# Kernel optimization log

Hardware: AMD Instinct MI355X
Metric: run time of the kernel (lower is better)

Reference implementation:

```python
import jax, jax.numpy as jnp
import numpy as np
from jax import lax

# Dimensions
B, CIN, COUT = 8, 3, 3
NF = 128          # num_features
K = 9             # DISCO kernel_shape (number of filter basis functions)
HLAT, WLON = 181, 360   # in_shape == out_shape (1-degree equiangular sphere grid)
KH, KW = 5, 5     # compact lat/lon support of each DISCO basis function


def setup_inputs() -> dict:
    key = jax.random.key(0)
    ks = jax.random.split(key, 10)
    s = lambda fan: 1.0 / np.sqrt(fan)
    return {
        "x": jax.random.normal(ks[0], (B, CIN, HLAT, WLON), jnp.float32),
        # DISCO conv: latitude-dependent basis filters, quadrature weights, channel mix
        "psi": jax.random.normal(ks[1], (K, HLAT, KH, KW), jnp.float32) * s(KH * KW),
        "quad": jnp.abs(jax.random.normal(ks[2], (HLAT,), jnp.float32)) * (1.0 / HLAT)
                + jnp.sin(jnp.pi * (jnp.arange(HLAT) + 0.5) / HLAT) * (1.0 / HLAT),
        "w1": jax.random.normal(ks[3], (NF, CIN, K), jnp.float32) * s(CIN * K),
        "b1": jnp.zeros((NF,), jnp.float32),
        # standard conv2d stages
        "w2": jax.random.normal(ks[4], (NF // 2, NF, 5, 5), jnp.float32) * s(NF * 25),
        "b2": jnp.zeros((NF // 2,), jnp.float32),
        "w3": jax.random.normal(ks[5], (COUT, NF // 2, 5, 5), jnp.float32) * s(NF // 2 * 25),
        "b3": jnp.zeros((COUT,), jnp.float32),
    }


def _disco_conv_s2(x, psi, quad, w, b):
    """Discrete-continuous spherical conv: latitude-dependent gather + weighted sum.
    x: [B,C,H,W]; psi: [K,H,KH,KW]; quad: [H]; w: [O,C,K]; b: [O] -> [B,O,H,W]"""
    H, W = x.shape[-2], x.shape[-1]
    rh, rw = KH // 2, KW // 2
    xw = x * quad[None, None, :, None]                       # quadrature-weighted input
    # neighborhood indices: clipped in latitude, circular in longitude
    hi = jnp.clip(jnp.arange(H)[:, None] + jnp.arange(KH)[None, :] - rh, 0, H - 1)  # [H,KH]
    wi = (jnp.arange(W)[:, None] + jnp.arange(KW)[None, :] - rw) % W                # [W,KW]
    g = xw[:, :, hi, :]                                      # [B,C,H,KH,W]
    patches = g[:, :, :, :, wi]                              # [B,C,H,KH,W,KW]
    # project onto latitude-dependent filter basis, then mix channels per basis
    z = jnp.einsum('khij,bchiwj->bckhw', psi, patches)       # [B,C,K,H,W]
    return jnp.einsum('ock,bckhw->bohw', w, z) + b[None, :, None, None]


def _conv2d(x, w, b, pad):
    y = lax.conv_general_dilated(x, w, (1, 1), [(pad, pad), (pad, pad)],
                                 dimension_numbers=('NCHW', 'OIHW', 'NCHW'))
    return y + b[None, :, None, None]


def reference(x, psi, quad, w1, b1, w2, b2, w3, b3):
    h = jax.nn.relu(_disco_conv_s2(x, psi, quad, w1, b1))
    h = jax.nn.relu(_conv2d(h, w2, b2, 2))
    return _conv2d(h, w3, b3, 2)
```

## Files before the change

kernel.cpp:

```cpp
#include <hip/hip_runtime.h>
#include <hip/hip_bf16.h>

#define HLAT 181
#define WLON 360
#define HW (HLAT * WLON)
#define HPAD 188
#define WPAD 368
#define PCH ((size_t)HPAD * WPAD * 16)
#define W2P 372
#define PLANE2 ((size_t)HPAD * W2P * 64)
#define ZROW ((size_t)12 * 4 * 32 * 16)

typedef __attribute__((ext_vector_type(4)))  short short4v;
typedef __attribute__((ext_vector_type(8)))  short short8v;
typedef __attribute__((ext_vector_type(4)))  float f32x4;
typedef __attribute__((ext_vector_type(16))) float f32x16;

static __device__ __forceinline__ ushort bf16_hi_bits(float f) {
  union { float f; unsigned u; } c; c.f = f;
  unsigned u = c.u;
  unsigned rounded = u + 0x7FFF + ((u >> 16) & 1);
  return (ushort)(rounded >> 16);
}
static __device__ __forceinline__ float bf16_to_f(ushort b) {
  union { unsigned u; float f; } c; c.u = ((unsigned)b) << 16;
  return c.f;
}

__global__ __launch_bounds__(256) void k_tw(const float* __restrict__ w2,
                                            const float* __restrict__ w3,
                                            const float* __restrict__ w1,
                                            const float* __restrict__ b1,
                                            ushort* __restrict__ w2f,
                                            ushort* __restrict__ w1f,
                                            ushort* __restrict__ w3f) {
  int idx = blockIdx.x * 256 + threadIdx.x;
  if (idx < 51200) {
    int l   = idx & 63;
    int p   = (idx >> 6) & 1;
    int m   = (idx >> 7) & 1;
    int ch  = (idx >> 8) & 7;
    int tap = idx >> 11;
    int oc  = m * 32 + (l & 31);
    int ci0 = ch * 16 + (l >> 5) * 8;
#pragma unroll
    for (int j = 0; j < 8; ++j) {
      float f = w2[(oc * 128 + ci0 + j) * 25 + tap];
      ushort hi = bf16_hi_bits(f);
      w2f[(size_t)idx * 8 + j] = (p == 0) ? hi : bf16_hi_bits(f - bf16_to_f(hi));
    }
  }
  if (idx < 1024) {
    int l = idx & 63;
    int e = idx >> 6;
    int p  = e & 1;
    int kc = (e >> 1) & 1;
    int m  = e >> 2;
    int oc = m * 32 + (l & 31);
    int k0 = kc * 16 + (l >> 5) * 8;
#pragma unroll
    for (int j = 0; j < 8; ++j) {
      int k = k0 + j;
      float f = (k < 27) ? w1[oc * 27 + k] : (k == 27 ? b1[oc] : 0.f);
      ushort hi = bf16_hi_bits(f);
      w1f[(size_t)idx * 8 + j] = (p == 0) ? hi : bf16_hi_bits(f - bf16_to_f(hi));
    }
  }
  if (idx < 6400) {
    int l   = idx & 63;
    int p   = (idx >> 6) & 1;
    int kc  = (idx >> 7) & 1;
    int tap = idx >> 8;
    int oc  = l & 15;
    int ci0 = kc * 32 + (l >> 4) * 8;
#pragma unroll
    for (int j = 0; j < 8; ++j) {
      float f = (oc < 3) ? w3[(oc * 64 + ci0 + j) * 25 + tap] : 0.f;
      ushort hi = bf16_hi_bits(f);
      w3f[(size_t)idx * 8 + j] = (p == 0) ? hi : bf16_hi_bits(f - bf16_to_f(hi));
    }
  }
}

__global__ __launch_bounds__(256) void k_zring(ushort* __restrict__ h1s) {
  const int i = blockIdx.x * 256 + threadIdx.x;
  if (i >= 4024) return;
  int row, col;
  if (i < 736)       { row = i / 368;              col = i % 368; }
  else if (i < 2576) { int p = i - 736;  row = 183 + p / 368; col = p % 368; }
  else if (i < 2938) { int p = i - 2576; row = 2 + p % 181;   col = p / 181; }
  else               { int p = i - 2938; row = 2 + p % 181;   col = 362 + p / 181; }
  short8v z = {0, 0, 0, 0, 0, 0, 0, 0};
  short8v* d = (short8v*)(h1s + (size_t)blockIdx.y * PCH + ((size_t)row * 368 + col) * 16);
  d[0] = z; d[1] = z;
}

__global__ __launch_bounds__(256) void k_zring2(ushort* __restrict__ h2p) {
  const int i = blockIdx.x * 256 + threadIdx.x;
  if (i >= 4776) return;
  int row, col;
  if (i < 744)       { row = i / W2P;             col = i % W2P; }
  else if (i < 2604) { int p = i - 744;  row = 183 + p / W2P; col = p % W2P; }
  else               { int p = i - 2604; row = 2 + p % 181;
                       int cI = p / 181; col = (cI < 2) ? cI : 360 + cI; }
  short8v z = {0, 0, 0, 0, 0, 0, 0, 0};
  short8v* d = (short8v*)(h2p + (size_t)blockIdx.y * PLANE2 + ((size_t)row * W2P + col) * 64);
#pragma unroll
  for (int k = 0; k < 8; ++k) d[k] = z;
}

__global__ __launch_bounds__(384, 2) void k_z(const float* __restrict__ x,
    const float* __restrict__ psi, const float* __restrict__ quad,
    ushort* __restrict__ zbuf, int b0) {
  const int h = blockIdx.x;
  const int bi = blockIdx.y;
  const int b = b0 + bi;
  const int tid = threadIdx.x;
  float z[28];
#pragma unroll
  for (int q = 0; q < 28; ++q) z[q] = 0.f;
  if (tid < 360) {
#pragma unroll 1
    for (int i = 0; i < 5; ++i) {
      int hi = h + i - 2;
      hi = hi < 0 ? 0 : (hi >= HLAT ? HLAT - 1 : hi);
      const float qv = quad[hi];
      float pv[45];
#pragma unroll
      for (int kk = 0; kk < 9; ++kk)
#pragma unroll
        for (int j = 0; j < 5; ++j)
          pv[kk * 5 + j] = psi[((size_t)(kk * HLAT + h)) * 25 + i * 5 + j];
#pragma unroll
      for (int c = 0; c < 3; ++c) {
        const float* row = x + ((size_t)(b * 3 + c) * HLAT + hi) * WLON;
        float v[5];
#pragma unroll
        for (int j = 0; j < 5; ++j) {
          int wj = tid + j - 2;
          wj = wj < 0 ? wj + WLON : (wj >= WLON ? wj - WLON : wj);
          v[j] = row[wj] * qv;
        }
#pragma unroll
        for (int kk = 0; kk < 9; ++kk) {
          float a = 0.f;
#pragma unroll
          for (int j = 0; j < 5; ++j) a += pv[kk * 5 + j] * v[j];
          z[c * 9 + kk] += a;
        }
      }
    }
    z[27] = 1.0f;
  }
  ushort hiv[32], lov[32];
#pragma unroll
  for (int q = 0; q < 28; ++q) {
    const ushort hb = bf16_hi_bits(z[q]);
    hiv[q] = hb;
    lov[q] = bf16_hi_bits(z[q] - bf16_to_f(hb));
  }
#pragma unroll
  for (int q = 28; q < 32; ++q) { hiv[q] = 0; lov[q] = 0; }

  ushort* tb = zbuf + (size_t)(bi * HLAT + h) * ZROW +
               (size_t)(tid >> 5) * 2048 + (size_t)(tid & 31) * 16;
#pragma unroll
  for (int pk = 0; pk < 4; ++pk) {
    const ushort* src = (pk < 2 ? hiv : lov) + (pk & 1) * 16;
    union { ushort u[8]; short8v v8; } a0, a1;
#pragma unroll
    for (int j = 0; j < 8; ++j) { a0.u[j] = src[j]; a1.u[j] = src[8 + j]; }
    *(short8v*)(tb + (size_t)pk * 512 + 0) = a0.v8;
    *(short8v*)(tb + (size_t)pk * 512 + 8) = a1.v8;
  }
}

__global__ __launch_bounds__(256, 2) void k_mv(const ushort* __restrict__ zbuf,
    const ushort* __restrict__ w1f, ushort* __restrict__ h1s) {
  __shared__ ushort st[4][16][32][16];
  const int h = blockIdx.x;
  const int bi = blockIdx.y;
  const int tid = threadIdx.x;
  const int wv = tid >> 6;
  const int l = tid & 63;
  const int l31 = l & 31;
  const int q = l >> 5;
  const short8v* wf1 = (const short8v*)w1f;
  short8v A[4][2][2];
#pragma unroll
  for (int m = 0; m < 4; ++m)
#pragma unroll
    for (int kc = 0; kc < 2; ++kc)
#pragma unroll
      for (int p = 0; p < 2; ++p)
        A[m][kc][p] = wf1[(size_t)(((m * 2 + kc) * 2 + p) * 64 + l)];

  ushort* base = h1s + (size_t)bi * 16 * PCH;
  const ushort* zrow = zbuf + (size_t)(bi * HLAT + h) * ZROW;
#pragma unroll
  for (int nn = 0; nn < 3; ++nn) {
    const int n = wv * 3 + nn;
    const ushort* zn = zrow + (size_t)n * 2048 + l31 * 16 + q * 8;
    const short8v bh0 = *(const short8v*)(zn + 0);
    const short8v bh1 = *(const short8v*)(zn + 512);
    const short8v bl0 = *(const short8v*)(zn + 1024);
    const short8v bl1 = *(const short8v*)(zn + 1536);
#pragma unroll
    for (int m = 0; m < 4; ++m) {
      f32x16 acc;
#pragma unroll
      for (int e = 0; e < 16; ++e) acc[e] = 0.f;
      acc = __builtin_amdgcn_mfma_f32_32x32x16_bf16(A[m][0][0], bh0, acc, 0, 0, 0);
      acc = __builtin_amdgcn_mfma_f32_32x32x16_bf16(A[m][0][1], bh0, acc, 0, 0, 0);
      acc = __builtin_amdgcn_mfma_f32_32x32x16_bf16(A[m][0][0], bl0, acc, 0, 0, 0);
      acc = __builtin_amdgcn_mfma_f32_32x32x16_bf16(A[m][1][0], bh1, acc, 0, 0, 0);
      acc = __builtin_amdgcn_mfma_f32_32x32x16_bf16(A[m][1][1], bh1, acc, 0, 0, 0);
      acc = __builtin_amdgcn_mfma_f32_32x32x16_bf16(A[m][1][0], bl1, acc, 0, 0, 0);
#pragma unroll
      for (int r = 0; r < 4; ++r) {
        const int rb = 8 * r + 4 * q;
        const int p2h = m * 2 + (rb >> 4);
        const int ci0 = rb & 15;
        short4v h4, l4;
#pragma unroll
        for (int j = 0; j < 4; ++j) {
          const float v = fmaxf(acc[r * 4 + j], 0.f);
          const ushort hb = bf16_hi_bits(v);
          h4[j] = (short)hb;
          l4[j] = (short)bf16_hi_bits(v - bf16_to_f(hb));
        }
        *(short4v*)&st[wv][p2h][l31][ci0] = h4;
        *(short4v*)&st[wv][8 + p2h][l31][ci0] = l4;
      }
    }
    const int pxr = n * 32 + (l >> 1);
    if (pxr < 360) {
      const size_t po = ((size_t)(h + 2) * WPAD + (pxr + 2)) * 16 + (l & 1) * 8;
#pragma unroll
      for (int p2 = 0; p2 < 16; ++p2) {
        const short8v v = *(const short8v*)&st[wv][p2][l >> 1][(l & 1) * 8];
        *(short8v*)(base + (size_t)p2 * PCH + po) = v;
      }
    }
  }
}

__global__ __launch_bounds__(256, 2) void k_conv2(const ushort* __restrict__ h1s,
    const ushort* __restrict__ w2f, const float* __restrict__ b2,
    ushort* __restrict__ h2p) {
  __shared__ ushort act[2][2][12][40][16];
  const int x0 = blockIdx.x * 32;
  const int y0 = blockIdx.y * 8;
  const int bi = blockIdx.z;
  const int tid = threadIdx.x;
  const int wv = tid >> 6;
  const int m  = wv >> 1;
  const int wr = wv & 1;
  const int l = tid & 63;
  const int l31 = l & 31;
  const int q8 = (l >> 5) * 8;

  f32x16 acc[4];
#pragma unroll
  for (int r = 0; r < 4; ++r)
#pragma unroll
    for (int e = 0; e < 16; ++e) acc[r][e] = 0.f;

  const short8v* wf = (const short8v*)w2f;
  const ushort* pbase = h1s + (size_t)bi * 16 * PCH;

  auto stage = [&](int buf, int ch) {
#pragma unroll
    for (int s = 0; s < 12; ++s) {
      const int k = wv * 12 + s;
      const int part = k / 24;
      const int rem = k - part * 24;
      const int t = rem >> 1;
      const int slot = rem & 1;
      const ushort* pl = pbase + (size_t)(part * 8 + ch) * PCH;
      if (slot == 0) {
        const ushort* g = pl + ((size_t)(y0 + t) * WPAD + (x0 + (l >> 1))) * 16 + (l & 1) * 8;
        __builtin_amdgcn_global_load_lds(
            (const __attribute__((address_space(1))) unsigned int*)g,
            (__attribute__((address_space(3))) unsigned int*)&act[buf][part][t][0][0], 16, 0, 0);
      } else {
        const ushort* g = pl + ((size_t)(y0 + t) * WPAD + (x0 + 32 + (l >> 3))) * 16 + (l & 7) * 2;
        __builtin_amdgcn_global_load_lds(
            (const __attribute__((address_space(1))) unsigned int*)g,
            (__attribute__((address_space(3))) unsigned int*)&act[buf][part][t][32][0], 4, 0, 0);
      }
    }
  };

  stage(0, 0);
  asm volatile("s_waitcnt vmcnt(0)" ::: "memory");
  __syncthreads();

#pragma unroll 1
  for (int ch = 0; ch < 8; ++ch) {
    const int cur = ch & 1;
    if (ch < 7) stage(cur ^ 1, ch + 1);
#pragma unroll 1
    for (int dj = 0; dj < 5; ++dj) {
      short8v aw[5][2];
#pragma unroll
      for (int di = 0; di < 5; ++di) {
        const size_t e0 = (size_t)(((di * 5 + dj) * 8 + ch) * 4 + m * 2) * 64 + l;
        aw[di][0] = wf[e0];
        aw[di][1] = wf[e0 + 64];
      }
      __builtin_amdgcn_s_setprio(1);
#pragma unroll
      for (int rr = 0; rr < 8; ++rr) {
        const int t = wr * 4 + rr;
        const int c = l31 + dj;
        const short8v bh = *(const short8v*)&act[cur][0][t][c][q8];
        const short8v bl = *(const short8v*)&act[cur][1][t][c][q8];
#pragma unroll
        for (int di = 0; di < 5; ++di) {
          const int r = rr - di;
          if (r < 0 || r > 3) continue;
          acc[r] = __builtin_amdgcn_mfma_f32_32x32x16_bf16(aw[di][0], bh, acc[r], 0, 0, 0);
          acc[r] = __builtin_amdgcn_mfma_f32_32x32x16_bf16(aw[di][1], bh, acc[r], 0, 0, 0);
          acc[r] = __builtin_amdgcn_mfma_f32_32x32x16_bf16(aw[di][0], bl, acc[r], 0, 0, 0);
        }
      }
      __builtin_amdgcn_s_setprio(0);
    }
    asm volatile("s_waitcnt vmcnt(0)" ::: "memory");
    __syncthreads();
  }

  const int xg = x0 + l31;
  ushort* hp = h2p + (size_t)bi * 2 * PLANE2;
  if (xg < WLON) {
#pragma unroll
    for (int r = 0; r < 4; ++r) {
      const int y = y0 + wr * 4 + r;
      if (y >= HLAT) continue;
      const size_t po = ((size_t)(y + 2) * W2P + (xg + 2)) * 64;
#pragma unroll
      for (int run = 0; run < 4; ++run) {
        const int oc0 = m * 32 + 8 * run + (q8 >> 1);
        short4v h4, l4;
#pragma unroll
        for (int j = 0; j < 4; ++j) {
          const float v = fmaxf(acc[r][run * 4 + j] + b2[oc0 + j], 0.f);
          const ushort hb = bf16_hi_bits(v);
          h4[j] = (short)hb;
          l4[j] = (short)bf16_hi_bits(v - bf16_to_f(hb));
        }
        *(short4v*)(hp + po + oc0) = h4;
        *(short4v*)(hp + PLANE2 + po + oc0) = l4;
      }
    }
  }
}

__global__ __launch_bounds__(256, 2) void k_conv3(const ushort* __restrict__ h2p,
    const ushort* __restrict__ w3f, const float* __restrict__ b3,
    float* __restrict__ out, int b0) {
  __shared__ ushort act[2][12][20][72];
  const int x0 = blockIdx.x * 16;
  const int y0 = blockIdx.y * 8;
  const int bi = blockIdx.z;
  const int tid = threadIdx.x;
  const int wv = tid >> 6;
  const int l = tid & 63;

  {
    const ushort* pb = h2p + (size_t)bi * 2 * PLANE2;
    float4 v[6][3];
#pragma unroll
    for (int pr = 0; pr < 6; ++pr) {
      const int pair = wv * 6 + pr;
      const int part = pair / 12;
      const int row = pair % 12;
      const ushort* src = pb + (size_t)part * PLANE2 +
                          ((size_t)(y0 + row) * W2P + x0) * 64;
      v[pr][0] = *(const float4*)((const char*)src + l * 16);
      v[pr][1] = *(const float4*)((const char*)src + 1024 + l * 16);
      if (l < 32) v[pr][2] = *(const float4*)((const char*)src + 2048 + l * 16);
    }
#pragma unroll
    for (int pr = 0; pr < 6; ++pr) {
      const int pair = wv * 6 + pr;
      const int part = pair / 12;
      const int row = pair % 12;
#pragma unroll
      for (int k2 = 0; k2 < 3; ++k2) {
        if (k2 == 2 && l >= 32) continue;
        const int B = k2 * 1024 + l * 16;
        const int col = B >> 7;
        const int ci = (B & 127) >> 1;
        *(short8v*)&act[part][row][col][ci] = *(short8v*)&v[pr][k2];
      }
    }
  }
  __syncthreads();

  f32x4 acc[2];
#pragma unroll
  for (int r = 0; r < 2; ++r)
#pragma unroll
    for (int e = 0; e < 4; ++e) acc[r][e] = 0.f;

  const short8v* wf3 = (const short8v*)w3f;
  const int c16 = l & 15;
  const int koff0 = ((l >> 4) & 3) * 8;

#pragma unroll 1
  for (int kc = 0; kc < 2; ++kc) {
#pragma unroll 1
    for (int dj = 0; dj < 5; ++dj) {
      short8v A[5][2];
#pragma unroll
      for (int di = 0; di < 5; ++di) {
        const size_t e0 = (size_t)(((di * 5 + dj) * 2 + kc) * 2) * 64 + l;
        A[di][0] = wf3[e0];
        A[di][1] = wf3[e0 + 64];
      }
      const int c = c16 + dj;
      const int koff = kc * 32 + koff0;
      __builtin_amdgcn_s_setprio(1);
#pragma unroll
      for (int tt = 0; tt < 6; ++tt) {
        const int t = wv * 2 + tt;
        const short8v bh = *(const short8v*)&act[0][t][c][koff];
        const short8v bl = *(const short8v*)&act[1][t][c][koff];
#pragma unroll
        for (int di = 0; di < 5; ++di) {
          const int r = tt - di;
          if (r < 0 || r > 1) continue;
          acc[r] = __builtin_amdgcn_mfma_f32_16x16x32_bf16(A[di][0], bh, acc[r], 0, 0, 0);
          acc[r] = __builtin_amdgcn_mfma_f32_16x16x32_bf16(A[di][1], bh, acc[r], 0, 0, 0);
          acc[r] = __builtin_amdgcn_mfma_f32_16x16x32_bf16(A[di][0], bl, acc[r], 0, 0, 0);
        }
      }
      __builtin_amdgcn_s_setprio(0);
    }
  }

  const int px = x0 + c16;
  const int b = b0 + bi;
  if ((l >> 4) == 0 && px < WLON) {
    const float bb[3] = {b3[0], b3[1], b3[2]};
#pragma unroll
    for (int r = 0; r < 2; ++r) {
      const int y = y0 + wv * 2 + r;
      if (y >= HLAT) continue;
#pragma unroll
      for (int j = 0; j < 3; ++j)
        out[((size_t)(b * 3 + j) * HLAT + y) * WLON + px] = acc[r][j] + bb[j];
    }
  }
}

extern "C" void kernel_launch(void* const* d_in, const int* in_sizes, int n_in,
                              void* d_out, int out_size, void* d_ws, size_t ws_size,
                              hipStream_t stream) {
  const float* x    = (const float*)d_in[0];
  const float* psi  = (const float*)d_in[1];
  const float* quad = (const float*)d_in[2];
  const float* w1   = (const float*)d_in[3];
  const float* b1   = (const float*)d_in[4];
  const float* w2   = (const float*)d_in[5];
  const float* b2   = (const float*)d_in[6];
  const float* w3   = (const float*)d_in[7];
  const float* b3   = (const float*)d_in[8];
  float* out = (float*)d_out;
  float* ws  = (float*)d_ws;

  ushort* w2f = (ushort*)ws;
  ushort* w1f = (ushort*)(ws + 204800);
  ushort* w3f = (ushort*)(ws + 208896);
  const size_t HEAD = 234496;

  size_t wsf = ws_size / 4;
  const size_t h1s_f = PCH * 8;
  const size_t h2p_f = PLANE2;
  const size_t per_b = h1s_f + h2p_f;
  int bc = 8;
  while (bc > 1 && HEAD + (size_t)bc * per_b > wsf) bc >>= 1;

  ushort* h1s = (ushort*)(ws + HEAD);
  ushort* h2p = (ushort*)(ws + HEAD + (size_t)bc * h1s_f);
  ushort* zbuf = h2p;

  k_tw<<<dim3(200), dim3(256), 0, stream>>>(w2, w3, w1, b1, w2f, w1f, w3f);
  k_zring<<<dim3(16, bc * 16), dim3(256), 0, stream>>>(h1s);

  for (int b0 = 0; b0 < 8; b0 += bc) {
    int cur = 8 - b0 < bc ? 8 - b0 : bc;
    k_z<<<dim3(HLAT, cur), dim3(384), 0, stream>>>(x, psi, quad, zbuf, b0);
    k_mv<<<dim3(HLAT, cur), dim3(256), 0, stream>>>(zbuf, w1f, h1s);
    k_zring2<<<dim3(19, cur * 2), dim3(256), 0, stream>>>(h2p);
    k_conv2<<<dim3(12, 23, cur), dim3(256), 0, stream>>>(h1s, w2f, b2, h2p);
    k_conv3<<<dim3(23, 23, cur), dim3(256), 0, stream>>>(h2p, w3f, b3, out, b0);
  }
}
```

Baseline: 756.9 us.

## Re-split conv2 warps by output rows and restage LDS with 16-byte loads

Each of the four waves in k_conv2 now computes both 32-channel output halves for two rows, instead of one half for four rows. That cuts the input-row halo each wave reads from LDS from 8 to 6 rows per output pair and reuses each B fragment across both weight blocks. Staging now uses a flat LDS layout filled only with 16-byte global_load_lds copies, with offsets precomputed per thread, which removes the 4-byte halo loads. The cost is doubled weight-fragment registers per wave, which may raise register pressure under the 256/2 launch bound.

New measurement: 821.2 us. +8.5%, slower.

```diff
diff --git a/kernel.cpp b/kernel.cpp
--- a/kernel.cpp
+++ b/kernel.cpp
@@ -248,46 +248,49 @@
 __global__ __launch_bounds__(256, 2) void k_conv2(const ushort* __restrict__ h1s,
     const ushort* __restrict__ w2f, const float* __restrict__ b2,
     ushort* __restrict__ h2p) {
-  __shared__ ushort act[2][2][12][40][16];
+  __shared__ ushort act[2][15360];
   const int x0 = blockIdx.x * 32;
   const int y0 = blockIdx.y * 8;
   const int bi = blockIdx.z;
   const int tid = threadIdx.x;
   const int wv = tid >> 6;
-  const int m  = wv >> 1;
-  const int wr = wv & 1;
   const int l = tid & 63;
   const int l31 = l & 31;
-  const int q8 = (l >> 5) * 8;
-
-  f32x16 acc[4];
-#pragma unroll
-  for (int r = 0; r < 4; ++r)
-#pragma unroll
-    for (int e = 0; e < 16; ++e) acc[r][e] = 0.f;
+  const int q = l >> 5;
+
+  f32x16 acc[2][2];
+#pragma unroll
+  for (int r = 0; r < 2; ++r)
+#pragma unroll
+    for (int m = 0; m < 2; ++m)
+#pragma unroll
+      for (int e = 0; e < 16; ++e) acc[r][m][e] = 0.f;
 
   const short8v* wf = (const short8v*)w2f;
   const ushort* pbase = h1s + (size_t)bi * 16 * PCH;
 
+  unsigned goff[8];
+#pragma unroll
+  for (int s = 0; s < 8; ++s) {
+    const int idx = (wv * 8 + s) * 64 + l;
+    const int reg = idx / 480;
+    const int rem = idx - reg * 480;
+    const int t = rem / 40;
+    const int c = rem - t * 40;
+    const int part = reg >> 1, qq = reg & 1;
+    goff[s] = (unsigned)(part * 8 * (unsigned)PCH) +
+              (unsigned)(((y0 + t) * WPAD + (x0 + c)) * 16 + qq * 8);
+  }
+
   auto stage = [&](int buf, int ch) {
 #pragma unroll
-    for (int s = 0; s < 12; ++s) {
-      const int k = wv * 12 + s;
-      const int part = k / 24;
-      const int rem = k - part * 24;
-      const int t = rem >> 1;
-      const int slot = rem & 1;
-      const ushort* pl = pbase + (size_t)(part * 8 + ch) * PCH;
-      if (slot == 0) {
-        const ushort* g = pl + ((size_t)(y0 + t) * WPAD + (x0 + (l >> 1))) * 16 + (l & 1) * 8;
+    for (int s = 0; s < 8; ++s) {
+      if (wv * 8 + s < 30) {
+        const ushort* g = pbase + (size_t)ch * PCH + goff[s];
+        ushort* d = &act[buf][(wv * 8 + s) * 512];
         __builtin_amdgcn_global_load_lds(
             (const __attribute__((address_space(1))) unsigned int*)g,
-            (__attribute__((address_space(3))) unsigned int*)&act[buf][part][t][0][0], 16, 0, 0);
-      } else {
-        const ushort* g = pl + ((size_t)(y0 + t) * WPAD + (x0 + 32 + (l >> 3))) * 16 + (l & 7) * 2;
-        __builtin_amdgcn_global_load_lds(
-            (const __attribute__((address_space(1))) unsigned int*)g,
-            (__attribute__((address_space(3))) unsigned int*)&act[buf][part][t][32][0], 4, 0, 0);
+            (__attribute__((address_space(3))) unsigned int*)d, 16, 0, 0);
       }
     }
   };
@@ -302,27 +305,33 @@
     if (ch < 7) stage(cur ^ 1, ch + 1);
 #pragma unroll 1
     for (int dj = 0; dj < 5; ++dj) {
-      short8v aw[5][2];
+      short8v aw[5][2][2];
 #pragma unroll
       for (int di = 0; di < 5; ++di) {
-        const size_t e0 = (size_t)(((di * 5 + dj) * 8 + ch) * 4 + m * 2) * 64 + l;
-        aw[di][0] = wf[e0];
-        aw[di][1] = wf[e0 + 64];
-      }
+        const size_t e0 = (size_t)(((di * 5 + dj) * 8 + ch) * 4) * 64 + l;
+#pragma unroll
+        for (int m = 0; m < 2; ++m) {
+          aw[di][0][m] = wf[e0 + (m * 2 + 0) * 64];
+          aw[di][1][m] = wf[e0 + (m * 2 + 1) * 64];
+        }
+      }
+      const unsigned rbase = q * 3840 + (l31 + dj) * 8;
       __builtin_amdgcn_s_setprio(1);
 #pragma unroll
-      for (int rr = 0; rr < 8; ++rr) {
-        const int t = wr * 4 + rr;
-        const int c = l31 + dj;
-        const short8v bh = *(const short8v*)&act[cur][0][t][c][q8];
-        const short8v bl = *(const short8v*)&act[cur][1][t][c][q8];
+      for (int rr = 0; rr < 6; ++rr) {
+        const int t = wv * 2 + rr;
+        const short8v bh = *(const short8v*)&act[cur][rbase + t * 320];
+        const short8v bl = *(const short8v*)&act[cur][7680 + rbase + t * 320];
 #pragma unroll
         for (int di = 0; di < 5; ++di) {
           const int r = rr - di;
-          if (r < 0 || r > 3) continue;
-          acc[r] = __builtin_amdgcn_mfma_f32_32x32x16_bf16(aw[di][0], bh, acc[r], 0, 0, 0);
-          acc[r] = __builtin_amdgcn_mfma_f32_32x32x16_bf16(aw[di][1], bh, acc[r], 0, 0, 0);
-          acc[r] = __builtin_amdgcn_mfma_f32_32x32x16_bf16(aw[di][0], bl, acc[r], 0, 0, 0);
+          if (r < 0 || r > 1) continue;
+#pragma unroll
+          for (int m = 0; m < 2; ++m) {
+            acc[r][m] = __builtin_amdgcn_mfma_f32_32x32x16_bf16(aw[di][0][m], bh, acc[r][m], 0, 0, 0);
+            acc[r][m] = __builtin_amdgcn_mfma_f32_32x32x16_bf16(aw[di][1][m], bh, acc[r][m], 0, 0, 0);
+            acc[r][m] = __builtin_amdgcn_mfma_f32_32x32x16_bf16(aw[di][0][m], bl, acc[r][m], 0, 0, 0);
+          }
         }
       }
       __builtin_amdgcn_s_setprio(0);
@@ -335,23 +344,26 @@
   ushort* hp = h2p + (size_t)bi * 2 * PLANE2;
   if (xg < WLON) {
 #pragma unroll
-    for (int r = 0; r < 4; ++r) {
-      const int y = y0 + wr * 4 + r;
+    for (int r = 0; r < 2; ++r) {
+      const int y = y0 + wv * 2 + r;
       if (y >= HLAT) continue;
       const size_t po = ((size_t)(y + 2) * W2P + (xg + 2)) * 64;
 #pragma unroll
-      for (int run = 0; run < 4; ++run) {
-        const int oc0 = m * 32 + 8 * run + (q8 >> 1);
-        short4v h4, l4;
-#pragma unroll
-        for (int j = 0; j < 4; ++j) {
-          const float v = fmaxf(acc[r][run * 4 + j] + b2[oc0 + j], 0.f);
-          const ushort hb = bf16_hi_bits(v);
-          h4[j] = (short)hb;
-          l4[j] = (short)bf16_hi_bits(v - bf16_to_f(hb));
-        }
-        *(short4v*)(hp + po + oc0) = h4;
-        *(short4v*)(hp + PLANE2 + po + oc0) = l4;
+      for (int m = 0; m < 2; ++m) {
+#pragma unroll
+        for (int run = 0; run < 4; ++run) {
+          const int oc0 = m * 32 + 8 * run + 4 * q;
+          short4v h4, l4;
+#pragma unroll
+          for (int j = 0; j < 4; ++j) {
+            const float v = fmaxf(acc[r][m][run * 4 + j] + b2[oc0 + j], 0.f);
+            const ushort hb = bf16_hi_bits(v);
+            h4[j] = (short)hb;
+            l4[j] = (short)bf16_hi_bits(v - bf16_to_f(hb));
+          }
+          *(short4v*)(hp + po + oc0) = h4;
+          *(short4v*)(hp + PLANE2 + po + oc0) = l4;
+        }
       }
     }
   }
```

## Split h1 planes into 8-channel halves so conv2 staging uses uniform 16-byte loads

Applied to the files above, without the earlier changes.

The intermediate h1 activation is now stored as 32 planes of 8 channels each instead of 16 planes of 16 channels. The k_mv writer, the zero-ring kernel and the conv2 staging all use the new layout. In conv2 the mixed 16-byte and 4-byte global_load_lds staging becomes uniform 16-byte loads with precomputed offsets, and the LDS tile is flattened to match. This removes the inefficient 4-byte halo loads and the per-stage index arithmetic. The cost is more distinct planes, with strided writes in k_mv and possibly less coalesced reads.

After: 763.1 us. No clear change (+0.8%).

```diff
diff --git a/kernel.cpp b/kernel.cpp
--- a/kernel.cpp
+++ b/kernel.cpp
@@ -6,7 +6,7 @@
 #define HW (HLAT * WLON)
 #define HPAD 188
 #define WPAD 368
-#define PCH ((size_t)HPAD * WPAD * 16)
+#define PCHH ((size_t)HPAD * WPAD * 8)
 #define W2P 372
 #define PLANE2 ((size_t)HPAD * W2P * 64)
 #define ZROW ((size_t)12 * 4 * 32 * 16)
@@ -91,8 +91,7 @@
   else if (i < 2938) { int p = i - 2576; row = 2 + p % 181;   col = p / 181; }
   else               { int p = i - 2938; row = 2 + p % 181;   col = 362 + p / 181; }
   short8v z = {0, 0, 0, 0, 0, 0, 0, 0};
-  short8v* d = (short8v*)(h1s + (size_t)blockIdx.y * PCH + ((size_t)row * 368 + col) * 16);
-  d[0] = z; d[1] = z;
+  *(short8v*)(h1s + (size_t)blockIdx.y * PCHH + ((size_t)row * 368 + col) * 8) = z;
 }
 
 __global__ __launch_bounds__(256) void k_zring2(ushort* __restrict__ h2p) {
@@ -195,7 +194,7 @@
       for (int p = 0; p < 2; ++p)
         A[m][kc][p] = wf1[(size_t)(((m * 2 + kc) * 2 + p) * 64 + l)];
 
-  ushort* base = h1s + (size_t)bi * 16 * PCH;
+  ushort* base = h1s + (size_t)bi * 32 * PCHH;
   const ushort* zrow = zbuf + (size_t)(bi * HLAT + h) * ZROW;
 #pragma unroll
   for (int nn = 0; nn < 3; ++nn) {
@@ -235,11 +234,11 @@
     }
     const int pxr = n * 32 + (l >> 1);
     if (pxr < 360) {
-      const size_t po = ((size_t)(h + 2) * WPAD + (pxr + 2)) * 16 + (l & 1) * 8;
+      const size_t po = ((size_t)(h + 2) * WPAD + (pxr + 2)) * 8;
 #pragma unroll
       for (int p2 = 0; p2 < 16; ++p2) {
         const short8v v = *(const short8v*)&st[wv][p2][l >> 1][(l & 1) * 8];
-        *(short8v*)(base + (size_t)p2 * PCH + po) = v;
+        *(short8v*)(base + (size_t)(p2 * 2 + (l & 1)) * PCHH + po) = v;
       }
     }
   }
@@ -248,7 +247,7 @@
 __global__ __launch_bounds__(256, 2) void k_conv2(const ushort* __restrict__ h1s,
     const ushort* __restrict__ w2f, const float* __restrict__ b2,
     ushort* __restrict__ h2p) {
-  __shared__ ushort act[2][2][12][40][16];
+  __shared__ ushort act[2][15360];
   const int x0 = blockIdx.x * 32;
   const int y0 = blockIdx.y * 8;
   const int bi = blockIdx.z;
@@ -258,7 +257,7 @@
   const int wr = wv & 1;
   const int l = tid & 63;
   const int l31 = l & 31;
-  const int q8 = (l >> 5) * 8;
+  const int q = l >> 5;
 
   f32x16 acc[4];
 #pragma unroll
@@ -267,27 +266,31 @@
     for (int e = 0; e < 16; ++e) acc[r][e] = 0.f;
 
   const short8v* wf = (const short8v*)w2f;
-  const ushort* pbase = h1s + (size_t)bi * 16 * PCH;
+  const ushort* pbase = h1s + (size_t)bi * 32 * PCHH;
+
+  unsigned goff[8];
+#pragma unroll
+  for (int s = 0; s < 8; ++s) {
+    const int idx = (wv * 8 + s) * 64 + l;
+    const int reg = idx / 480;
+    const int rem = idx - reg * 480;
+    const int t = rem / 40;
+    const int c = rem - t * 40;
+    const int part = reg >> 1, qq = reg & 1;
+    goff[s] = (unsigned)((part * 16 + qq) * PCHH) +
+              (unsigned)(((y0 + t) * WPAD + (x0 + c)) * 8);
+  }
 
   auto stage = [&](int buf, int ch) {
-#pragma unroll
-    for (int s = 0; s < 12; ++s) {
-      const int k = wv * 12 + s;
-      const int part = k / 24;
-      const int rem = k - part * 24;
-      const int t = rem >> 1;
-      const int slot = rem & 1;
-      const ushort* pl = pbase + (size_t)(part * 8 + ch) * PCH;
-      if (slot == 0) {
-        const ushort* g = pl + ((size_t)(y0 + t) * WPAD + (x0 + (l >> 1))) * 16 + (l & 1) * 8;
+    const size_t choff = (size_t)ch * 2 * PCHH;
+#pragma unroll
+    for (int s = 0; s < 8; ++s) {
+      if (wv * 8 + s < 30) {
+        const ushort* g = pbase + choff + goff[s];
+        ushort* d = &act[buf][(wv * 8 + s) * 512];
         __builtin_amdgcn_global_load_lds(
             (const __attribute__((address_space(1))) unsigned int*)g,
-            (__attribute__((address_space(3))) unsigned int*)&act[buf][part][t][0][0], 16, 0, 0);
-      } else {
-        const ushort* g = pl + ((size_t)(y0 + t) * WPAD + (x0 + 32 + (l >> 3))) * 16 + (l & 7) * 2;
-        __builtin_amdgcn_global_load_lds(
-            (const __attribute__((address_space(1))) unsigned int*)g,
-            (__attribute__((address_space(3))) unsigned int*)&act[buf][part][t][32][0], 4, 0, 0);
+            (__attribute__((address_space(3))) unsigned int*)d, 16, 0, 0);
       }
     }
   };
@@ -309,13 +312,13 @@
         aw[di][0] = wf[e0];
         aw[di][1] = wf[e0 + 64];
       }
+      const unsigned rbase = q * 3840 + (l31 + dj) * 8;
       __builtin_amdgcn_s_setprio(1);
 #pragma unroll
       for (int rr = 0; rr < 8; ++rr) {
         const int t = wr * 4 + rr;
-        const int c = l31 + dj;
-        const short8v bh = *(const short8v*)&act[cur][0][t][c][q8];
-        const short8v bl = *(const short8v*)&act[cur][1][t][c][q8];
+        const short8v bh = *(const short8v*)&act[cur][rbase + t * 320];
+        const short8v bl = *(const short8v*)&act[cur][7680 + rbase + t * 320];
 #pragma unroll
         for (int di = 0; di < 5; ++di) {
           const int r = rr - di;
@@ -341,7 +344,7 @@
       const size_t po = ((size_t)(y + 2) * W2P + (xg + 2)) * 64;
 #pragma unroll
       for (int run = 0; run < 4; ++run) {
-        const int oc0 = m * 32 + 8 * run + (q8 >> 1);
+        const int oc0 = m * 32 + 8 * run + 4 * q;
         short4v h4, l4;
 #pragma unroll
         for (int j = 0; j < 4; ++j) {
@@ -477,7 +480,7 @@
   const size_t HEAD = 234496;
 
   size_t wsf = ws_size / 4;
-  const size_t h1s_f = PCH * 8;
+  const size_t h1s_f = PCHH * 16;
   const size_t h2p_f = PLANE2;
   const size_t per_b = h1s_f + h2p_f;
   int bc = 8;
@@ -488,7 +491,7 @@
   ushort* zbuf = h2p;
 
   k_tw<<<dim3(200), dim3(256), 0, stream>>>(w2, w3, w1, b1, w2f, w1f, w3f);
-  k_zring<<<dim3(16, bc * 16), dim3(256), 0, stream>>>(h1s);
+  k_zring<<<dim3(16, bc * 32), dim3(256), 0, stream>>>(h1s);
 
   for (int b0 = 0; b0 < 8; b0 += bc) {
     int cur = 8 - b0 < bc ? 8 - b0 : bc;
```
